# Kernel optimization log

Hardware: AMD Instinct MI355X
Metric: run time of the kernel (lower is better)

Reference implementation:

```python
import jax, jax.numpy as jnp
import numpy as np

HEADS = 16
HEAD_DIM = 64
EMBED = HEADS * HEAD_DIM  # 1024
B, S = 2, 2048


def setup_inputs() -> dict:
    key = jax.random.key(0)
    ks = jax.random.split(key, 9)
    return {
        "value": jax.random.normal(ks[0], (B, S, EMBED), dtype=jnp.float32),
        "key": jax.random.normal(ks[1], (B, S, EMBED), dtype=jnp.float32),
        "query": jax.random.normal(ks[2], (B, S, EMBED), dtype=jnp.float32),
        "mask": jax.random.randint(ks[3], (B, 1, S, S), 0, 2, dtype=jnp.int32),
        "Wq": jax.random.normal(ks[4], (HEAD_DIM, HEAD_DIM), dtype=jnp.float32) * 0.02,
        "Wk": jax.random.normal(ks[5], (HEAD_DIM, HEAD_DIM), dtype=jnp.float32) * 0.02,
        "Wv": jax.random.normal(ks[6], (HEAD_DIM, HEAD_DIM), dtype=jnp.float32) * 0.02,
        "Wo": jax.random.normal(ks[7], (EMBED, EMBED), dtype=jnp.float32) * 0.02,
        "bo": jnp.zeros((EMBED,), dtype=jnp.float32),
    }


def reference(value, key, query, mask, Wq, Wk, Wv, Wo, bo):
    N, Lv = value.shape[0], value.shape[1]
    Lk, Lq = key.shape[1], query.shape[1]
    # Faithful to original: plain reshape (N, heads, len, head_dim), NOT transpose.
    v = value.reshape(N, HEADS, Lv, HEAD_DIM)
    k = key.reshape(N, HEADS, Lk, HEAD_DIM)
    q = query.reshape(N, HEADS, Lq, HEAD_DIM)
    # Per-head Linear (no bias): x @ W.T
    V = jnp.einsum('bhld,ed->bhle', v, Wv)
    K = jnp.einsum('bhld,ed->bhle', k, Wk)
    Q = jnp.einsum('bhld,ed->bhle', q, Wq)
    score = jnp.einsum('bhqd,bhkd->bhqk', Q, K)  # [B,H,Sq,Sk]
    score = jnp.where(mask == 0, jnp.float32(-1e20), score)
    # Faithful quirk: scale by sqrt(embed_size), not sqrt(head_dim)
    scale = jnp.float32(EMBED ** 0.5)
    attn = jax.nn.softmax(score / scale, axis=3)
    out = jnp.einsum('bhqk,bhkd->bhqd', attn, V).reshape(N, Lq, HEADS * HEAD_DIM)
    return out @ Wo.T + bo
```

## Files before the change

kernel.cpp:

```cpp
#include <hip/hip_runtime.h>
#include <hip/hip_bf16.h>
#include <cstdint>
#include <cstddef>

#define S_LEN 2048
#define N_HEADS 16
#define HD 64
#define EMB 1024
#define N_BATCH 2
#define N_BH (N_BATCH * N_HEADS)

typedef __attribute__((ext_vector_type(4))) float f32x4;
typedef __attribute__((ext_vector_type(8))) short short8;
typedef __attribute__((ext_vector_type(8))) _Float16 half8;
typedef __attribute__((ext_vector_type(2))) unsigned uint2v;
typedef __attribute__((ext_vector_type(4))) unsigned uint4v;

__device__ __forceinline__ f32x4 mfma16h(half8 a, half8 b, f32x4 c) {
    return __builtin_amdgcn_mfma_f32_16x16x32_f16(a, b, c, 0, 0, 0);
}

__device__ __forceinline__ unsigned pkh(float a, float b) {
    return __builtin_bit_cast(unsigned, __builtin_amdgcn_cvt_pkrtz(a, b));
}

#if __has_builtin(__builtin_amdgcn_exp2f)
__device__ __forceinline__ float fast_exp2(float x) { return __builtin_amdgcn_exp2f(x); }
#else
__device__ __forceinline__ float fast_exp2(float x) { return exp2f(x); }
#endif

__global__ __launch_bounds__(256) void prep_kernel(
    const float* __restrict__ q_in, const float* __restrict__ k_in,
    const float* __restrict__ v_in,
    const float* __restrict__ Wq, const float* __restrict__ Wk,
    const float* __restrict__ Wv, const float* __restrict__ Wo,
    const int* __restrict__ mask,
    short* __restrict__ Qb, short* __restrict__ Kb, short* __restrict__ Vt,
    short* __restrict__ Woh, unsigned long long* __restrict__ bits) {
    __shared__ short Al[64 * 72];
    __shared__ short Wl[64 * 72];
    __shared__ short Ol[64 * 72];
    int bx = blockIdx.x;
    int t = threadIdx.x;

    if (bx >= 3072) {
        if (bx < 11264) {
            int wid = ((bx - 3072) * 256 + t) >> 6;
            int lane = t & 63;
            const int* src = mask + (size_t)wid * 256 + lane;
            unsigned long long w0 = __ballot(src[0] != 0);
            unsigned long long w1 = __ballot(src[64] != 0);
            unsigned long long w2 = __ballot(src[128] != 0);
            unsigned long long w3 = __ballot(src[192] != 0);
            if (lane == 0) {
                unsigned long long* dst = bits + (size_t)wid * 4;
                dst[0] = w0; dst[1] = w1; dst[2] = w2; dst[3] = w3;
            }
        } else {
            int i = (bx - 11264) * 256 + t;
            f32x4 a = reinterpret_cast<const f32x4*>(Wo)[i * 2];
            f32x4 b = reinterpret_cast<const f32x4*>(Wo)[i * 2 + 1];
            uint4 u = { pkh(a.x, a.y), pkh(a.z, a.w), pkh(b.x, b.y), pkh(b.z, b.w) };
            reinterpret_cast<uint4*>(Woh)[i] = u;
        }
        return;
    }

    int rt = bx & 31;
    int bh = (bx >> 5) & 31;
    int tz = bx >> 10;
    const float* src = (tz == 0 ? q_in : tz == 1 ? k_in : v_in)
                       + (size_t)bh * S_LEN * HD + (size_t)rt * 64 * HD;
    const float* W = (tz == 0 ? Wq : tz == 1 ? Wk : Wv);

#pragma unroll
    for (int r = 0; r < 4; r++) {
        int f4 = t + 256 * r;
        int row = f4 >> 4;
        int c4 = (f4 & 15) * 4;
        f32x4 a = reinterpret_cast<const f32x4*>(src)[f4];
        uint2 ua = { pkh(a.x, a.y), pkh(a.z, a.w) };
        *reinterpret_cast<uint2*>(&Al[row * 72 + c4]) = ua;
        f32x4 w = reinterpret_cast<const f32x4*>(W)[f4];
        uint2 uw = { pkh(w.x, w.y), pkh(w.z, w.w) };
        *reinterpret_cast<uint2*>(&Wl[row * 72 + c4]) = uw;
    }
    __syncthreads();

    int wave = t >> 6, lane = t & 63, quad = lane >> 4, col = lane & 15;
    half8 a0 = *reinterpret_cast<const half8*>(&Al[(wave * 16 + col) * 72 + quad * 8]);
    half8 a1 = *reinterpret_cast<const half8*>(&Al[(wave * 16 + col) * 72 + 32 + quad * 8]);

    const float C1 = 0.04508422002777448f;
    float scl = (tz == 0) ? C1 : 1.0f;

    f32x4 acc[4];
#pragma unroll
    for (int jt = 0; jt < 4; jt++) {
        half8 b0 = *reinterpret_cast<const half8*>(&Wl[(jt * 16 + col) * 72 + quad * 8]);
        half8 b1 = *reinterpret_cast<const half8*>(&Wl[(jt * 16 + col) * 72 + 32 + quad * 8]);
        f32x4 c = {0.f, 0.f, 0.f, 0.f};
        c = mfma16h(a0, b0, c);
        c = mfma16h(a1, b1, c);
        acc[jt] = c;
    }
    __syncthreads();

    if (tz < 2) {
#pragma unroll
        for (int jt = 0; jt < 4; jt++)
#pragma unroll
            for (int i = 0; i < 4; i++)
                Ol[(wave * 16 + quad * 4 + i) * 72 + jt * 16 + col] =
                    __builtin_bit_cast(short, (_Float16)(acc[jt][i] * scl));
        __syncthreads();
        short* dst = (tz == 0 ? Qb : Kb) + (size_t)bh * S_LEN * HD + (size_t)rt * 64 * HD;
        int row = t >> 2, ck = (t & 3) * 16;
        short8 o0 = *reinterpret_cast<const short8*>(&Ol[row * 72 + ck]);
        short8 o1 = *reinterpret_cast<const short8*>(&Ol[row * 72 + ck + 8]);
        *reinterpret_cast<short8*>(&dst[row * 64 + ck]) = o0;
        *reinterpret_cast<short8*>(&dst[row * 64 + ck + 8]) = o1;
    } else {
#pragma unroll
        for (int jt = 0; jt < 4; jt++)
#pragma unroll
            for (int i = 0; i < 4; i++)
                Ol[(jt * 16 + col) * 72 + wave * 16 + quad * 4 + i] =
                    __builtin_bit_cast(short, (_Float16)acc[jt][i]);
        __syncthreads();
        short* dst = Vt + (size_t)bh * HD * S_LEN + rt * 64;
        int d = t >> 2, ck = (t & 3) * 16;
        short8 o0 = *reinterpret_cast<const short8*>(&Ol[d * 72 + ck]);
        short8 o1 = *reinterpret_cast<const short8*>(&Ol[d * 72 + ck + 8]);
        *reinterpret_cast<short8*>(&dst[(size_t)d * S_LEN + ck]) = o0;
        *reinterpret_cast<short8*>(&dst[(size_t)d * S_LEN + ck + 8]) = o1;
    }
}

__global__ __launch_bounds__(512, 4) void attn_kernel(
    const short* __restrict__ Qb, const short* __restrict__ Kb,
    const short* __restrict__ Vt, const unsigned long long* __restrict__ mbits,
    short* __restrict__ Xb) {
    int qt = blockIdx.x;
    int bh = blockIdx.y;
    int b = bh >> 4;
    int t = threadIdx.x, wave = t >> 6, lane = t & 63, quad = lane >> 4, col = lane & 15;
    int qg = wave & 3;
    int par = wave >> 2;

    __shared__ short smem[32768];

    const short* Qh = Qb + (size_t)bh * S_LEN * HD;
    const short* Kh = Kb + (size_t)bh * S_LEN * HD;
    const short* Vh = Vt + (size_t)bh * HD * S_LEN;
    int q0 = qt * 128 + qg * 32;

    half8 qf00 = *reinterpret_cast<const half8*>(&Qh[(size_t)(q0 + col) * HD + quad * 8]);
    half8 qf01 = *reinterpret_cast<const half8*>(&Qh[(size_t)(q0 + col) * HD + 32 + quad * 8]);
    half8 qf10 = *reinterpret_cast<const half8*>(&Qh[(size_t)(q0 + 16 + col) * HD + quad * 8]);
    half8 qf11 = *reinterpret_cast<const half8*>(&Qh[(size_t)(q0 + 16 + col) * HD + 32 + quad * 8]);

    const unsigned long long* mrow0 = mbits + (size_t)(b * S_LEN + q0 + col) * 32;
    const unsigned long long* mrow1 = mbits + (size_t)(b * S_LEN + q0 + 16 + col) * 32;

    int r0 = t >> 3, cc = t & 7;
    int dst0 = r0 * 64 + ((cc ^ (r0 & 7)) * 8);
    int ch0 = cc & ~1;
    int h4 = (cc & 1) * 4;
    int vdA = r0 * 64 + ((ch0 ^ (r0 & 7)) * 8) + h4;
    int vdB = r0 * 64 + (((ch0 + 1) ^ (r0 & 7)) * 8) + h4;
    const short* kg0 = Kh + r0 * HD + cc * 8;
    const short* vg0 = Vh + (size_t)r0 * S_LEN + cc * 8;

    {
        short8 a = *reinterpret_cast<const short8*>(kg0);
        short8 b2 = *reinterpret_cast<const short8*>(kg0 + 4096);
        uint4v uc = __builtin_bit_cast(uint4v, *reinterpret_cast<const short8*>(vg0));
        uint4v ud = __builtin_bit_cast(uint4v, *reinterpret_cast<const short8*>(vg0 + 64));
        *reinterpret_cast<short8*>(&smem[dst0]) = a;
        *reinterpret_cast<short8*>(&smem[8192 + dst0]) = b2;
        *reinterpret_cast<uint2v*>(&smem[16384 + vdA]) = (uint2v){uc.x, uc.y};
        *reinterpret_cast<uint2v*>(&smem[16384 + vdB]) = (uint2v){uc.z, uc.w};
        *reinterpret_cast<uint2v*>(&smem[24576 + vdA]) = (uint2v){ud.x, ud.y};
        *reinterpret_cast<uint2v*>(&smem[24576 + vdB]) = (uint2v){ud.z, ud.w};
    }
    __syncthreads();

    unsigned bs[4];
#pragma unroll
    for (int i = 0; i < 4; i++) bs[i] = 1u << (quad * 4 + i);
    half8 ones = { (_Float16)1.f, (_Float16)1.f, (_Float16)1.f, (_Float16)1.f,
                   (_Float16)1.f, (_Float16)1.f, (_Float16)1.f, (_Float16)1.f };

    int sw = quad ^ (col & 7);
    unsigned long long mw0 = mrow0[par];
    unsigned long long mw1 = mrow1[par];

    f32x4 o[4][2];
    f32x4 l0 = {0.f, 0.f, 0.f, 0.f}, l1 = {0.f, 0.f, 0.f, 0.f};
#pragma unroll
    for (int dt = 0; dt < 4; dt++) {
        o[dt][0] = (f32x4){0.f, 0.f, 0.f, 0.f};
        o[dt][1] = (f32x4){0.f, 0.f, 0.f, 0.f};
    }

    int rdoff = 0;
    for (int s = 0; s < 16; s++) {
        int wroff = rdoff ^ 4096;
        const short* Kp = smem + par * 8192 + rdoff;
        const short* Vp = smem + 16384 + par * 8192 + rdoff;
        short8 pk0, pk1, pv0, pv1;
        unsigned long long mn0, mn1;
        if (s < 15) {
            pk0 = *reinterpret_cast<const short8*>(kg0 + (2 * s + 2) * 4096);
            pk1 = *reinterpret_cast<const short8*>(kg0 + (2 * s + 3) * 4096);
            pv0 = *reinterpret_cast<const short8*>(vg0 + (2 * s + 2) * 64);
            pv1 = *reinterpret_cast<const short8*>(vg0 + (2 * s + 3) * 64);
            mn0 = mrow0[2 * s + 2 + par];
            mn1 = mrow1[2 * s + 2 + par];
        }
        unsigned wA[4][2], wB[4][2];
#pragma unroll
        for (int mt = 0; mt < 4; mt++) {
            const short* kbase = &Kp[(mt * 16 + col) * 64];
            half8 ka0 = *reinterpret_cast<const half8*>(&kbase[sw * 8]);
            half8 ka1 = *reinterpret_cast<const half8*>(&kbase[(sw ^ 4) * 8]);
            f32x4 c0 = {0.f, 0.f, 0.f, 0.f};
            f32x4 c1 = {0.f, 0.f, 0.f, 0.f};
            c0 = mfma16h(ka0, qf00, c0);
            c0 = mfma16h(ka1, qf01, c0);
            c1 = mfma16h(ka0, qf10, c1);
            c1 = mfma16h(ka1, qf11, c1);
            unsigned g0 = (unsigned)(mw0 >> (mt * 16));
            unsigned g1 = (unsigned)(mw1 >> (mt * 16));
            float p00 = fast_exp2((g0 & bs[0]) ? c0[0] : -200.0f);
            float p01 = fast_exp2((g0 & bs[1]) ? c0[1] : -200.0f);
            float p02 = fast_exp2((g0 & bs[2]) ? c0[2] : -200.0f);
            float p03 = fast_exp2((g0 & bs[3]) ? c0[3] : -200.0f);
            wA[mt][0] = pkh(p00, p01);
            wA[mt][1] = pkh(p02, p03);
            float p10 = fast_exp2((g1 & bs[0]) ? c1[0] : -200.0f);
            float p11 = fast_exp2((g1 & bs[1]) ? c1[1] : -200.0f);
            float p12 = fast_exp2((g1 & bs[2]) ? c1[2] : -200.0f);
            float p13 = fast_exp2((g1 & bs[3]) ? c1[3] : -200.0f);
            wB[mt][0] = pkh(p10, p11);
            wB[mt][1] = pkh(p12, p13);
        }
#pragma unroll
        for (int c = 0; c < 2; c++) {
            auto ra0 = __builtin_amdgcn_permlane32_swap(wA[2 * c][0], wA[2 * c + 1][0], false, false);
            auto ra1 = __builtin_amdgcn_permlane32_swap(wA[2 * c][1], wA[2 * c + 1][1], false, false);
            auto rb0 = __builtin_amdgcn_permlane32_swap(wB[2 * c][0], wB[2 * c + 1][0], false, false);
            auto rb1 = __builtin_amdgcn_permlane32_swap(wB[2 * c][1], wB[2 * c + 1][1], false, false);
            half8 pb0 = __builtin_bit_cast(half8, (uint4v){ra0[0], ra1[0], ra0[1], ra1[1]});
            half8 pb1 = __builtin_bit_cast(half8, (uint4v){rb0[0], rb1[0], rb0[1], rb1[1]});
            l0 = mfma16h(ones, pb0, l0);
            l1 = mfma16h(ones, pb1, l1);
#pragma unroll
            for (int dt = 0; dt < 4; dt++) {
                half8 va = *reinterpret_cast<const half8*>(
                    &Vp[(dt * 16 + col) * 64 + (((c * 4 + quad) ^ (col & 7)) * 8)]);
                o[dt][0] = mfma16h(va, pb0, o[dt][0]);
                o[dt][1] = mfma16h(va, pb1, o[dt][1]);
            }
        }
        if (s < 15) {
            uint4v u0 = __builtin_bit_cast(uint4v, pv0);
            uint4v u1 = __builtin_bit_cast(uint4v, pv1);
            *reinterpret_cast<short8*>(&smem[wroff + dst0]) = pk0;
            *reinterpret_cast<short8*>(&smem[8192 + wroff + dst0]) = pk1;
            *reinterpret_cast<uint2v*>(&smem[16384 + wroff + vdA]) = (uint2v){u0.x, u0.y};
            *reinterpret_cast<uint2v*>(&smem[16384 + wroff + vdB]) = (uint2v){u0.z, u0.w};
            *reinterpret_cast<uint2v*>(&smem[24576 + wroff + vdA]) = (uint2v){u1.x, u1.y};
            *reinterpret_cast<uint2v*>(&smem[24576 + wroff + vdB]) = (uint2v){u1.z, u1.w};
            mw0 = mn0;
            mw1 = mn1;
        }
        __syncthreads();
        rdoff = wroff;
    }

    float* Obuf = (float*)smem;
    short* Ps = smem + 16384;
    float* Lbuf = (float*)(smem + 25600);
    if (par == 1) {
        float* ob = Obuf + qg * 2048 + lane * 32;
#pragma unroll
        for (int dt = 0; dt < 4; dt++) {
            *reinterpret_cast<f32x4*>(&ob[((dt * 2 + 0) ^ (lane & 7)) * 4]) = o[dt][0];
            *reinterpret_cast<f32x4*>(&ob[((dt * 2 + 1) ^ (lane & 7)) * 4]) = o[dt][1];
        }
        if (quad == 0) {
            Lbuf[qg * 32 + col] = l0[0];
            Lbuf[qg * 32 + 16 + col] = l1[0];
        }
    }
    __syncthreads();
    if (par == 0) {
        short* Pw = Ps + qg * (32 * 72);
        float* ob = Obuf + qg * 2048 + lane * 32;
        float inv0 = 1.0f / (l0[0] + Lbuf[qg * 32 + col]);
        float inv1 = 1.0f / (l1[0] + Lbuf[qg * 32 + 16 + col]);
#pragma unroll
        for (int dt = 0; dt < 4; dt++) {
            f32x4 a0 = *reinterpret_cast<const f32x4*>(&ob[((dt * 2 + 0) ^ (lane & 7)) * 4]);
            f32x4 a1 = *reinterpret_cast<const f32x4*>(&ob[((dt * 2 + 1) ^ (lane & 7)) * 4]);
            float v00 = (o[dt][0][0] + a0.x) * inv0, v01 = (o[dt][0][1] + a0.y) * inv0;
            float v02 = (o[dt][0][2] + a0.z) * inv0, v03 = (o[dt][0][3] + a0.w) * inv0;
            float v10 = (o[dt][1][0] + a1.x) * inv1, v11 = (o[dt][1][1] + a1.y) * inv1;
            float v12 = (o[dt][1][2] + a1.z) * inv1, v13 = (o[dt][1][3] + a1.w) * inv1;
            uint2 dw0 = { pkh(v00, v01), pkh(v02, v03) };
            uint2 dw1 = { pkh(v10, v11), pkh(v12, v13) };
            *reinterpret_cast<uint2*>(&Pw[col * 72 + dt * 16 + quad * 4]) = dw0;
            *reinterpret_cast<uint2*>(&Pw[(16 + col) * 72 + dt * 16 + quad * 4]) = dw1;
        }
        int rr = lane >> 2, ckk = (lane & 3) * 16;
        short* Xrow = Xb + (size_t)bh * S_LEN * HD + (size_t)(q0 + rr) * HD;
        short8 x0 = *reinterpret_cast<const short8*>(&Pw[rr * 72 + ckk]);
        short8 x1 = *reinterpret_cast<const short8*>(&Pw[rr * 72 + ckk + 8]);
        *reinterpret_cast<short8*>(&Xrow[ckk]) = x0;
        *reinterpret_cast<short8*>(&Xrow[ckk + 8]) = x1;
        short* Xrow2 = Xrow + 16 * HD;
        short8 y0 = *reinterpret_cast<const short8*>(&Pw[(16 + rr) * 72 + ckk]);
        short8 y1 = *reinterpret_cast<const short8*>(&Pw[(16 + rr) * 72 + ckk + 8]);
        *reinterpret_cast<short8*>(&Xrow2[ckk]) = y0;
        *reinterpret_cast<short8*>(&Xrow2[ckk + 8]) = y1;
    }
}

__global__ __launch_bounds__(256, 4) void final_kernel(
    const short* __restrict__ Xb, const short* __restrict__ Woh,
    const float* __restrict__ bo, float* __restrict__ out) {
    int nb = blockIdx.x;
    int mb = blockIdx.y;
    int t = threadIdx.x, wave = t >> 6, lane = t & 63, quad = lane >> 4, col = lane & 15;
    __shared__ short Xs[128 * 64];
    __shared__ short Ws[64 * 64];

    int m0 = mb * 128, n0 = nb * 64;
    int r0 = t >> 3, cc = t & 7;

    int dstX[4], dstW[2];
    const short* xg[4];
    const short* wg[2];
#pragma unroll
    for (int u = 0; u < 4; u++) {
        int row = r0 + u * 32;
        dstX[u] = row * 64 + ((cc ^ (row & 7)) * 8);
        xg[u] = Xb + (size_t)(m0 + row) * EMB + cc * 8;
    }
#pragma unroll
    for (int u = 0; u < 2; u++) {
        int row = r0 + u * 32;
        dstW[u] = row * 64 + ((cc ^ (row & 7)) * 8);
        wg[u] = Woh + (size_t)(n0 + row) * EMB + cc * 8;
    }

    short8 px[4], pw[2];
#pragma unroll
    for (int u = 0; u < 4; u++) px[u] = *reinterpret_cast<const short8*>(xg[u]);
#pragma unroll
    for (int u = 0; u < 2; u++) pw[u] = *reinterpret_cast<const short8*>(wg[u]);
#pragma unroll
    for (int u = 0; u < 4; u++) *reinterpret_cast<short8*>(&Xs[dstX[u]]) = px[u];
#pragma unroll
    for (int u = 0; u < 2; u++) *reinterpret_cast<short8*>(&Ws[dstW[u]]) = pw[u];
    __syncthreads();

    int sw = quad ^ (col & 7);
    f32x4 acc[2][4];
#pragma unroll
    for (int mf = 0; mf < 2; mf++)
#pragma unroll
        for (int nf = 0; nf < 4; nf++) acc[mf][nf] = (f32x4){0.f, 0.f, 0.f, 0.f};

    for (int s = 0; s < 16; s++) {
        if (s < 15) {
#pragma unroll
            for (int u = 0; u < 4; u++)
                px[u] = *reinterpret_cast<const short8*>(xg[u] + (s + 1) * 64);
#pragma unroll
            for (int u = 0; u < 2; u++)
                pw[u] = *reinterpret_cast<const short8*>(wg[u] + (s + 1) * 64);
        }
        const short* ar0 = &Xs[(wave * 32 + col) * 64];
        const short* ar1 = &Xs[(wave * 32 + 16 + col) * 64];
        half8 a00 = *reinterpret_cast<const half8*>(&ar0[sw * 8]);
        half8 a01 = *reinterpret_cast<const half8*>(&ar0[(sw ^ 4) * 8]);
        half8 a10 = *reinterpret_cast<const half8*>(&ar1[sw * 8]);
        half8 a11 = *reinterpret_cast<const half8*>(&ar1[(sw ^ 4) * 8]);
#pragma unroll
        for (int nf = 0; nf < 4; nf++) {
            const short* br = &Ws[(nf * 16 + col) * 64];
            half8 b0 = *reinterpret_cast<const half8*>(&br[sw * 8]);
            half8 b1 = *reinterpret_cast<const half8*>(&br[(sw ^ 4) * 8]);
            acc[0][nf] = mfma16h(a00, b0, acc[0][nf]);
            acc[0][nf] = mfma16h(a01, b1, acc[0][nf]);
            acc[1][nf] = mfma16h(a10, b0, acc[1][nf]);
            acc[1][nf] = mfma16h(a11, b1, acc[1][nf]);
        }
        __syncthreads();
        if (s < 15) {
#pragma unroll
            for (int u = 0; u < 4; u++) *reinterpret_cast<short8*>(&Xs[dstX[u]]) = px[u];
#pragma unroll
            for (int u = 0; u < 2; u++) *reinterpret_cast<short8*>(&Ws[dstW[u]]) = pw[u];
            __syncthreads();
        }
    }

    float bb[4];
#pragma unroll
    for (int nf = 0; nf < 4; nf++) bb[nf] = bo[n0 + nf * 16 + col];
#pragma unroll
    for (int mf = 0; mf < 2; mf++)
#pragma unroll
        for (int i = 0; i < 4; i++) {
            int row = m0 + wave * 32 + mf * 16 + quad * 4 + i;
            float* orow = out + (size_t)row * EMB + n0;
#pragma unroll
            for (int nf = 0; nf < 4; nf++)
                orow[nf * 16 + col] = acc[mf][nf][i] + bb[nf];
        }
}

extern "C" void kernel_launch(void* const* d_in, const int* in_sizes, int n_in,
                              void* d_out, int out_size, void* d_ws, size_t ws_size,
                              hipStream_t stream) {
    const float* value = (const float*)d_in[0];
    const float* key_  = (const float*)d_in[1];
    const float* query = (const float*)d_in[2];
    const int*   mask  = (const int*)d_in[3];
    const float* Wq = (const float*)d_in[4];
    const float* Wk = (const float*)d_in[5];
    const float* Wv = (const float*)d_in[6];
    const float* Wo = (const float*)d_in[7];
    const float* bo = (const float*)d_in[8];
    float* out = (float*)d_out;

    char* ws = (char*)d_ws;
    short* Qb  = (short*)(ws);
    short* Kb  = (short*)(ws + (size_t)8  * 1048576);
    short* Vt  = (short*)(ws + (size_t)16 * 1048576);
    short* Xb  = (short*)(ws + (size_t)24 * 1048576);
    short* Woh = (short*)(ws + (size_t)32 * 1048576);
    unsigned long long* mbits =
        (unsigned long long*)(ws + (size_t)34 * 1048576);

    prep_kernel<<<dim3(3072 + 8192 + 512), dim3(256), 0, stream>>>(
        query, key_, value, Wq, Wk, Wv, Wo, mask, Qb, Kb, Vt, Woh, mbits);
    attn_kernel<<<dim3(S_LEN / 128, N_BH), dim3(512), 0, stream>>>(Qb, Kb, Vt, mbits, Xb);
    final_kernel<<<dim3(EMB / 64, (N_BATCH * S_LEN) / 128), dim3(256), 0, stream>>>(
        Xb, Woh, bo, out);
}
```

Measured before the change: 204.0 us.

## Load K/V tiles directly into LDS via global_load_lds with pre-permuted V layout

Replaces the register-staged K/V prefetch (global load to VGPRs, then LDS store) with direct global-to-LDS DMA loads. The needed swizzle now comes from permuting source addresses per lane. To let V land in the required interleaved layout with contiguous 16-byte copies, the prep kernel rewrites Vt with half-chunks swapped. This removes the VGPR pressure and LDS store instructions from the attention loop, but it relies on the async loads being complete at the barrier, and it couples the two kernels through the new V storage layout.

```diff
diff --git a/kernel.cpp b/kernel.cpp
--- a/kernel.cpp
+++ b/kernel.cpp
@@ -29,6 +29,12 @@
 #else
 __device__ __forceinline__ float fast_exp2(float x) { return exp2f(x); }
 #endif
+
+__device__ __forceinline__ void gl2lds16(const short* g, short* l) {
+    __builtin_amdgcn_global_load_lds(
+        (const __attribute__((address_space(1))) void*)g,
+        (__attribute__((address_space(3))) void*)l, 16, 0, 0);
+}
 
 __global__ __launch_bounds__(256) void prep_kernel(
     const float* __restrict__ q_in, const float* __restrict__ k_in,
@@ -133,8 +139,12 @@
         int d = t >> 2, ck = (t & 3) * 16;
         short8 o0 = *reinterpret_cast<const short8*>(&Ol[d * 72 + ck]);
         short8 o1 = *reinterpret_cast<const short8*>(&Ol[d * 72 + ck + 8]);
-        *reinterpret_cast<short8*>(&dst[(size_t)d * S_LEN + ck]) = o0;
-        *reinterpret_cast<short8*>(&dst[(size_t)d * S_LEN + ck + 8]) = o1;
+        uint4v u0 = __builtin_bit_cast(uint4v, o0);
+        uint4v u1 = __builtin_bit_cast(uint4v, o1);
+        short8 n0 = __builtin_bit_cast(short8, (uint4v){u0.x, u0.y, u1.x, u1.y});
+        short8 n1 = __builtin_bit_cast(short8, (uint4v){u0.z, u0.w, u1.z, u1.w});
+        *reinterpret_cast<short8*>(&dst[(size_t)d * S_LEN + ck]) = n0;
+        *reinterpret_cast<short8*>(&dst[(size_t)d * S_LEN + ck + 8]) = n1;
     }
 }
 
@@ -164,28 +174,20 @@
     const unsigned long long* mrow0 = mbits + (size_t)(b * S_LEN + q0 + col) * 32;
     const unsigned long long* mrow1 = mbits + (size_t)(b * S_LEN + q0 + 16 + col) * 32;
 
-    int r0 = t >> 3, cc = t & 7;
-    int dst0 = r0 * 64 + ((cc ^ (r0 & 7)) * 8);
-    int ch0 = cc & ~1;
-    int h4 = (cc & 1) * 4;
-    int vdA = r0 * 64 + ((ch0 ^ (r0 & 7)) * 8) + h4;
-    int vdB = r0 * 64 + (((ch0 + 1) ^ (r0 & 7)) * 8) + h4;
-    const short* kg0 = Kh + r0 * HD + cc * 8;
-    const short* vg0 = Vh + (size_t)r0 * S_LEN + cc * 8;
-
-    {
-        short8 a = *reinterpret_cast<const short8*>(kg0);
-        short8 b2 = *reinterpret_cast<const short8*>(kg0 + 4096);
-        uint4v uc = __builtin_bit_cast(uint4v, *reinterpret_cast<const short8*>(vg0));
-        uint4v ud = __builtin_bit_cast(uint4v, *reinterpret_cast<const short8*>(vg0 + 64));
-        *reinterpret_cast<short8*>(&smem[dst0]) = a;
-        *reinterpret_cast<short8*>(&smem[8192 + dst0]) = b2;
-        *reinterpret_cast<uint2v*>(&smem[16384 + vdA]) = (uint2v){uc.x, uc.y};
-        *reinterpret_cast<uint2v*>(&smem[16384 + vdB]) = (uint2v){uc.z, uc.w};
-        *reinterpret_cast<uint2v*>(&smem[24576 + vdA]) = (uint2v){ud.x, ud.y};
-        *reinterpret_cast<uint2v*>(&smem[24576 + vdB]) = (uint2v){ud.z, ud.w};
-    }
-    __syncthreads();
+    int lrow = lane >> 3;
+    int lsw = (lane & 7) ^ lrow;
+    int grow = wave * 8 + lrow;
+    const short* kp0 = Kh + grow * 64 + lsw * 8;
+    const short* vp0 = Vh + (size_t)grow * S_LEN + lsw * 8;
+    short* kl0 = smem + wave * 512;
+    short* kl1 = smem + 8192 + wave * 512;
+    short* vl0 = smem + 16384 + wave * 512;
+    short* vl1 = smem + 24576 + wave * 512;
+
+    gl2lds16(kp0, kl0);
+    gl2lds16(kp0 + 4096, kl1);
+    gl2lds16(vp0, vl0);
+    gl2lds16(vp0 + 64, vl1);
 
     unsigned bs[4];
 #pragma unroll
@@ -204,22 +206,24 @@
         o[dt][0] = (f32x4){0.f, 0.f, 0.f, 0.f};
         o[dt][1] = (f32x4){0.f, 0.f, 0.f, 0.f};
     }
-
-    int rdoff = 0;
+    __syncthreads();
+
     for (int s = 0; s < 16; s++) {
-        int wroff = rdoff ^ 4096;
-        const short* Kp = smem + par * 8192 + rdoff;
-        const short* Vp = smem + 16384 + par * 8192 + rdoff;
-        short8 pk0, pk1, pv0, pv1;
+        int rd = (s & 1) * 4096;
+        int wr = 4096 - rd;
         unsigned long long mn0, mn1;
         if (s < 15) {
-            pk0 = *reinterpret_cast<const short8*>(kg0 + (2 * s + 2) * 4096);
-            pk1 = *reinterpret_cast<const short8*>(kg0 + (2 * s + 3) * 4096);
-            pv0 = *reinterpret_cast<const short8*>(vg0 + (2 * s + 2) * 64);
-            pv1 = *reinterpret_cast<const short8*>(vg0 + (2 * s + 3) * 64);
+            const short* ka = kp0 + (2 * s + 2) * 4096;
+            const short* va = vp0 + (2 * s + 2) * 64;
+            gl2lds16(ka, kl0 + wr);
+            gl2lds16(ka + 4096, kl1 + wr);
+            gl2lds16(va, vl0 + wr);
+            gl2lds16(va + 64, vl1 + wr);
             mn0 = mrow0[2 * s + 2 + par];
             mn1 = mrow1[2 * s + 2 + par];
         }
+        const short* Kp = smem + par * 8192 + rd;
+        const short* Vp = smem + 16384 + par * 8192 + rd;
         unsigned wA[4][2], wB[4][2];
 #pragma unroll
         for (int mt = 0; mt < 4; mt++) {
@@ -266,19 +270,10 @@
             }
         }
         if (s < 15) {
-            uint4v u0 = __builtin_bit_cast(uint4v, pv0);
-            uint4v u1 = __builtin_bit_cast(uint4v, pv1);
-            *reinterpret_cast<short8*>(&smem[wroff + dst0]) = pk0;
-            *reinterpret_cast<short8*>(&smem[8192 + wroff + dst0]) = pk1;
-            *reinterpret_cast<uint2v*>(&smem[16384 + wroff + vdA]) = (uint2v){u0.x, u0.y};
-            *reinterpret_cast<uint2v*>(&smem[16384 + wroff + vdB]) = (uint2v){u0.z, u0.w};
-            *reinterpret_cast<uint2v*>(&smem[24576 + wroff + vdA]) = (uint2v){u1.x, u1.y};
-            *reinterpret_cast<uint2v*>(&smem[24576 + wroff + vdB]) = (uint2v){u1.z, u1.w};
             mw0 = mn0;
             mw1 = mn1;
         }
         __syncthreads();
-        rdoff = wroff;
     }
 
     float* Obuf = (float*)smem;
```

New measurement: 193.9 us. -5.0%, faster.
